# Kernel optimization log

Measured on AMD Instinct MI355X. Metric: run time of the kernel, lower is better.

## Reference

```python
import jax, jax.numpy as jnp
import numpy as np


def setup_inputs() -> dict:
    key = jax.random.key(0)
    k1, k2, k3, k4 = jax.random.split(key, 4)
    B, S, D, Y = 8, 2048, 512, 8921
    # xavier_uniform scale for [Y, D] weights
    lim = float(np.sqrt(6.0 / (Y + D)))
    x = jax.random.normal(k1, (B, S, D), dtype=jnp.float32)
    U_w = jax.random.uniform(k2, (Y, D), minval=-lim, maxval=lim, dtype=jnp.float32)
    final_w = jax.random.uniform(k3, (Y, D), minval=-lim, maxval=lim, dtype=jnp.float32)
    final_b = jax.random.normal(k4, (Y,), dtype=jnp.float32) * 0.02
    return {"x": x, "U_w": U_w, "final_w": final_w, "final_b": final_b}


def reference(x, U_w, final_w, final_b):
    # att: [B, Y, S] = U_w @ x^T
    att = jnp.einsum("yd,bsd->bys", U_w, x)
    alpha = jax.nn.softmax(att, axis=2)          # softmax over sequence
    m = jnp.einsum("bys,bsd->byd", alpha, x)      # per-label context [B, Y, D]
    y = jnp.einsum("yd,byd->by", final_w, m) + final_b  # [B, Y]
    return y
```

## Files before the change

### kernel.cpp

```cpp
#include <hip/hip_runtime.h>
#include <hip/hip_bf16.h>

constexpr int B_ = 8;
constexpr int S_ = 2048;
constexpr int D_ = 512;
constexpr int Y_ = 8921;
constexpr int MT_ = 70;
constexpr int SG_ = 4;

typedef __attribute__((ext_vector_type(8))) __bf16 bf16x8;
typedef __attribute__((ext_vector_type(4))) float f32x4;

__device__ __forceinline__ int swz_el(int row, int ksel8) {
  return row * 64 + ((ksel8 ^ row) & 7) * 8;
}

__global__ __launch_bounds__(256) void cvtW(const float* __restrict__ U,
                                            const float* __restrict__ F,
                                            __hip_bfloat16* __restrict__ wsW) {
  const int c = blockIdx.x * 256 + threadIdx.x;
  const int tile = c >> 11;
  const int row = (c >> 3) & 255;
  const int cs = c & 7;
  const int mt = tile >> 3, kt = tile & 7;
  const int ch = cs ^ (row & 7);
  const int g = row >> 5, h = (row >> 4) & 1, w = row & 15;
  const int y = mt * 128 + g * 16 + w;
  float4 f0 = {0.f, 0.f, 0.f, 0.f}, f1 = {0.f, 0.f, 0.f, 0.f};
  if (y < Y_) {
    const float* src = (h ? F : U) + (size_t)y * D_ + kt * 64 + ch * 8;
    f0 = reinterpret_cast<const float4*>(src)[0];
    f1 = reinterpret_cast<const float4*>(src)[1];
  }
  bf16x8 v;
  v[0] = (__bf16)f0.x; v[1] = (__bf16)f0.y; v[2] = (__bf16)f0.z; v[3] = (__bf16)f0.w;
  v[4] = (__bf16)f1.x; v[5] = (__bf16)f1.y; v[6] = (__bf16)f1.z; v[7] = (__bf16)f1.w;
  *reinterpret_cast<bf16x8*>(wsW + (size_t)c * 8) = v;
}

__global__ __launch_bounds__(256) void cvtX(const float* __restrict__ x,
                                            __hip_bfloat16* __restrict__ wsX) {
  const int c = blockIdx.x * 256 + threadIdx.x;
  const int lane = c & 63;
  const int idx2 = (c >> 6) & 7;
  const int wn = (c >> 9) & 3;
  const int kt = (c >> 11) & 7;
  const int st = (c >> 14) & 7;
  const int b = (c >> 17) & 7;
  const int n = idx2 >> 1, kk = idx2 & 1;
  const int s = st * 256 + wn * 64 + n * 16 + (lane & 15);
  const int k = kt * 64 + kk * 32 + (lane >> 4) * 8;
  const float* src = x + ((size_t)b * S_ + s) * D_ + k;
  const float4 f0 = reinterpret_cast<const float4*>(src)[0];
  const float4 f1 = reinterpret_cast<const float4*>(src)[1];
  bf16x8 v;
  v[0] = (__bf16)f0.x; v[1] = (__bf16)f0.y; v[2] = (__bf16)f0.z; v[3] = (__bf16)f0.w;
  v[4] = (__bf16)f1.x; v[5] = (__bf16)f1.y; v[6] = (__bf16)f1.z; v[7] = (__bf16)f1.w;
  *reinterpret_cast<bf16x8*>(wsX + (size_t)c * 8) = v;
}

__global__ __launch_bounds__(256) void zeroLN(float* __restrict__ LN, int n) {
  const int i = blockIdx.x * 256 + threadIdx.x;
  if (i < n) LN[i] = 0.f;
}

__global__ __launch_bounds__(256) void combine(const float* __restrict__ Lg,
                                               const float* __restrict__ Ng,
                                               const float* __restrict__ fb,
                                               float* __restrict__ out) {
  const int y = blockIdx.x * 256 + threadIdx.x;
  const int b = blockIdx.y;
  if (y < Y_) out[(size_t)b * Y_ + y] = Ng[b * Y_ + y] / Lg[b * Y_ + y] + fb[y];
}

typedef const __attribute__((address_space(1))) void gv_t;
typedef __attribute__((address_space(3))) void lv_t;

__device__ __forceinline__ void gld_lds16(const void* g, void* l) {
  __builtin_amdgcn_global_load_lds((gv_t*)g, (lv_t*)l, 16, 0, 0);
}

__global__ __launch_bounds__(512, 2) void pool_main(
    const __hip_bfloat16* __restrict__ wsW, const __hip_bfloat16* __restrict__ wsX,
    float* __restrict__ Lg, float* __restrict__ Ng) {
  const int bid = blockIdx.x;
  const int b = bid & 7;
  const int r = bid >> 3;
  const int mt = r % MT_;
  const int sg = r / MT_;

  const int tid = threadIdx.x;
  const int lane = tid & 63;
  const int wid = tid >> 6;
  const int wm = wid >> 2;
  const int wn = wid & 3;
  const int l15 = lane & 15;
  const int l4 = lane >> 4;

  __shared__ __bf16 ldsA[2 * 16384];
  __shared__ float redL[128];
  __shared__ float redN[128];

  if (tid < 128) { redL[tid] = 0.f; redN[tid] = 0.f; }

  const __bf16* Wbase = (const __bf16*)wsW + (size_t)mt * 8 * 16384;
  const __bf16* xc = (const __bf16*)wsX +
      ((size_t)(b * 8 + sg * 2) * 8) * 16384 + wn * 4096 + lane * 8;

  f32x4 acc[8][4];
  bf16x8 X0[4], X1[4];

  auto stageA = [&](int ktn, int par) {
    const char* src = (const char*)(Wbase + ktn * 16384) + (wid * 256 + lane) * 16;
    char* dst = (char*)ldsA + par * 32768 + wid * 4096;
#pragma unroll
    for (int i = 0; i < 4; ++i)
      gld_lds16(src + i * 1024, dst + i * 1024);
  };

  stageA(0, 0);
#pragma unroll
  for (int n = 0; n < 4; ++n)
    X0[n] = *reinterpret_cast<const bf16x8*>(xc + n * 1024);
  asm volatile("s_waitcnt vmcnt(0) lgkmcnt(0)" ::: "memory");
  __builtin_amdgcn_s_barrier();
  __builtin_amdgcn_sched_barrier(0);

  for (int si = 0; si < 2; ++si) {
#pragma unroll
    for (int m = 0; m < 8; ++m)
#pragma unroll
      for (int n = 0; n < 4; ++n) acc[m][n] = (f32x4){0.f, 0.f, 0.f, 0.f};

    for (int kt = 0; kt < 8; ++kt) {
      const __bf16* A = ldsA + ((kt & 1) << 14);
      const bool has_next = !(si == 1 && kt == 7);

      {
        bf16x8 af[4];
#pragma unroll
        for (int j = 0; j < 4; ++j)
          af[j] = *reinterpret_cast<const bf16x8*>(
              &A[swz_el(wm * 128 + j * 16 + l15, l4)]);
#pragma unroll
        for (int n = 0; n < 4; ++n)
          X1[n] = *reinterpret_cast<const bf16x8*>(xc + n * 1024 + 512);
        if (has_next) stageA((kt + 1) & 7, (kt + 1) & 1);
        __builtin_amdgcn_s_barrier();
        __builtin_amdgcn_s_setprio(1);
#pragma unroll
        for (int j = 0; j < 4; ++j)
#pragma unroll
          for (int n = 0; n < 4; ++n)
            acc[j][n] = __builtin_amdgcn_mfma_f32_16x16x32_bf16(af[j], X0[n], acc[j][n], 0, 0, 0);
        __builtin_amdgcn_s_setprio(0);
        __builtin_amdgcn_s_barrier();
      }
      {
        bf16x8 af[4];
#pragma unroll
        for (int j = 0; j < 4; ++j)
          af[j] = *reinterpret_cast<const bf16x8*>(
              &A[swz_el(wm * 128 + (4 + j) * 16 + l15, l4)]);
        __builtin_amdgcn_s_barrier();
        __builtin_amdgcn_s_setprio(1);
#pragma unroll
        for (int j = 0; j < 4; ++j)
#pragma unroll
          for (int n = 0; n < 4; ++n)
            acc[4 + j][n] = __builtin_amdgcn_mfma_f32_16x16x32_bf16(af[j], X0[n], acc[4 + j][n], 0, 0, 0);
        __builtin_amdgcn_s_setprio(0);
        __builtin_amdgcn_s_barrier();
      }
      {
        bf16x8 af[4];
#pragma unroll
        for (int j = 0; j < 4; ++j)
          af[j] = *reinterpret_cast<const bf16x8*>(
              &A[swz_el(wm * 128 + j * 16 + l15, 4 + l4)]);
        if (has_next) {
#pragma unroll
          for (int n = 0; n < 4; ++n)
            X0[n] = *reinterpret_cast<const bf16x8*>(xc + 16384 + n * 1024);
        }
        __builtin_amdgcn_s_barrier();
        __builtin_amdgcn_s_setprio(1);
#pragma unroll
        for (int j = 0; j < 4; ++j)
#pragma unroll
          for (int n = 0; n < 4; ++n)
            acc[j][n] = __builtin_amdgcn_mfma_f32_16x16x32_bf16(af[j], X1[n], acc[j][n], 0, 0, 0);
        __builtin_amdgcn_s_setprio(0);
        __builtin_amdgcn_s_barrier();
      }
      {
        bf16x8 af[4];
#pragma unroll
        for (int j = 0; j < 4; ++j)
          af[j] = *reinterpret_cast<const bf16x8*>(
              &A[swz_el(wm * 128 + (4 + j) * 16 + l15, 4 + l4)]);
        __builtin_amdgcn_s_barrier();
        __builtin_amdgcn_s_setprio(1);
#pragma unroll
        for (int j = 0; j < 4; ++j)
#pragma unroll
          for (int n = 0; n < 4; ++n)
            acc[4 + j][n] = __builtin_amdgcn_mfma_f32_16x16x32_bf16(af[j], X1[n], acc[4 + j][n], 0, 0, 0);
        __builtin_amdgcn_s_setprio(0);
        asm volatile("s_waitcnt vmcnt(0)" ::: "memory");
        __builtin_amdgcn_s_barrier();
        __builtin_amdgcn_sched_barrier(0);
      }
      xc += 16384;
    }

#pragma unroll
    for (int g = 0; g < 4; ++g)
#pragma unroll
      for (int q = 0; q < 4; ++q) {
        float l = 0.f, nn = 0.f;
#pragma unroll
        for (int n = 0; n < 4; ++n) {
          const float e = __expf(acc[2 * g][n][q]);
          l += e;
          nn = fmaf(e, acc[2 * g + 1][n][q], nn);
        }
#pragma unroll
        for (int mask = 1; mask <= 8; mask <<= 1) {
          l += __shfl_xor(l, mask);
          nn += __shfl_xor(nn, mask);
        }
        if (l15 == 0) {
          const int yl = wm * 64 + g * 16 + (l4 << 2) + q;
          atomicAdd(&redL[yl], l);
          atomicAdd(&redN[yl], nn);
        }
      }
  }

  __syncthreads();
  if (tid < 128) {
    const int y = mt * 128 + tid;
    if (y < Y_) {
      atomicAdd(&Lg[(size_t)b * Y_ + y], redL[tid]);
      atomicAdd(&Ng[(size_t)b * Y_ + y], redN[tid]);
    }
  }
}

constexpr int FB_BY = 128, FB_BS = 64, FB_BK = 64;

__device__ __forceinline__ int fswz(int row, int k) {
  return row * FB_BK + ((((k >> 3) ^ row) & 7) << 3) + (k & 7);
}

template <int CHUNKS>
__device__ __forceinline__ void fb_stage(const float* __restrict__ gbase, int rstride,
                                         int maxrow, __bf16* lds, int tid) {
#pragma unroll
  for (int i = 0; i < CHUNKS / 256; ++i) {
    const int c = tid + 256 * i;
    const int row = c >> 3;
    const int ch = c & 7;
    float4 f0 = {0.f, 0.f, 0.f, 0.f}, f1 = {0.f, 0.f, 0.f, 0.f};
    if (row < maxrow) {
      const float4* p = reinterpret_cast<const float4*>(gbase + (size_t)row * rstride + ch * 8);
      f0 = p[0]; f1 = p[1];
    }
    bf16x8 v;
    v[0] = (__bf16)f0.x; v[1] = (__bf16)f0.y; v[2] = (__bf16)f0.z; v[3] = (__bf16)f0.w;
    v[4] = (__bf16)f1.x; v[5] = (__bf16)f1.y; v[6] = (__bf16)f1.z; v[7] = (__bf16)f1.w;
    *reinterpret_cast<bf16x8*>(&lds[fswz(row, ch * 8)]) = v;
  }
}

__global__ __launch_bounds__(256) void output_layer_fallback(
    const float* __restrict__ x, const float* __restrict__ Uw,
    const float* __restrict__ Fw, const float* __restrict__ fb,
    float* __restrict__ out) {
  const int b = blockIdx.y;
  const int y0 = blockIdx.x * FB_BY;
  const int tid = threadIdx.x;
  const int lane = tid & 63;
  const int w = tid >> 6;
  const int wm = (w >> 1) * 64, wn = (w & 1) * 32;
  __shared__ __bf16 sU[FB_BY * FB_BK], sF[FB_BY * FB_BK], sX[FB_BS * FB_BK];
  float Ls[4][4], Ns[4][4];
#pragma unroll
  for (int m = 0; m < 4; ++m)
#pragma unroll
    for (int q = 0; q < 4; ++q) { Ls[m][q] = 0.f; Ns[m][q] = 0.f; }
  const float* xb = x + (size_t)b * S_ * D_;
  const int umax = Y_ - y0;
  for (int s0 = 0; s0 < S_; s0 += FB_BS) {
    f32x4 accA[4][2] = {}, accP[4][2] = {};
    for (int k0 = 0; k0 < D_; k0 += FB_BK) {
      __syncthreads();
      fb_stage<FB_BY * 8>(Uw + (size_t)y0 * D_ + k0, D_, umax, sU, tid);
      fb_stage<FB_BY * 8>(Fw + (size_t)y0 * D_ + k0, D_, umax, sF, tid);
      fb_stage<FB_BS * 8>(xb + (size_t)s0 * D_ + k0, D_, FB_BS, sX, tid);
      __syncthreads();
#pragma unroll
      for (int kk = 0; kk < 2; ++kk) {
        const int kb = kk * 32 + (lane >> 4) * 8;
        bf16x8 bx[2];
#pragma unroll
        for (int n = 0; n < 2; ++n)
          bx[n] = *reinterpret_cast<const bf16x8*>(&sX[fswz(wn + n * 16 + (lane & 15), kb)]);
#pragma unroll
        for (int m = 0; m < 4; ++m) {
          const bf16x8 aU = *reinterpret_cast<const bf16x8*>(&sU[fswz(wm + m * 16 + (lane & 15), kb)]);
          const bf16x8 aF = *reinterpret_cast<const bf16x8*>(&sF[fswz(wm + m * 16 + (lane & 15), kb)]);
#pragma unroll
          for (int n = 0; n < 2; ++n) {
            accA[m][n] = __builtin_amdgcn_mfma_f32_16x16x32_bf16(aU, bx[n], accA[m][n], 0, 0, 0);
            accP[m][n] = __builtin_amdgcn_mfma_f32_16x16x32_bf16(aF, bx[n], accP[m][n], 0, 0, 0);
          }
        }
      }
    }
#pragma unroll
    for (int m = 0; m < 4; ++m)
#pragma unroll
      for (int n = 0; n < 2; ++n)
#pragma unroll
        for (int q = 0; q < 4; ++q) {
          const float e = __expf(accA[m][n][q]);
          Ls[m][q] += e;
          Ns[m][q] = fmaf(e, accP[m][n][q], Ns[m][q]);
        }
  }
  __syncthreads();
  float* redL = reinterpret_cast<float*>(sU);
  float* redN = reinterpret_cast<float*>(sF);
  for (int i = tid; i < FB_BY; i += 256) { redL[i] = 0.f; redN[i] = 0.f; }
  __syncthreads();
#pragma unroll
  for (int m = 0; m < 4; ++m)
#pragma unroll
    for (int q = 0; q < 4; ++q) {
      float l = Ls[m][q], nn = Ns[m][q];
#pragma unroll
      for (int mask = 1; mask <= 8; mask <<= 1) {
        l += __shfl_xor(l, mask);
        nn += __shfl_xor(nn, mask);
      }
      if ((lane & 15) == 0) {
        const int yl = wm + m * 16 + ((lane >> 4) << 2) + q;
        atomicAdd(&redL[yl], l);
        atomicAdd(&redN[yl], nn);
      }
    }
  __syncthreads();
  for (int i = tid; i < FB_BY; i += 256) {
    const int y = y0 + i;
    if (y < Y_) out[(size_t)b * Y_ + y] = redN[i] / redL[i] + fb[y];
  }
}

extern "C" void kernel_launch(void* const* d_in, const int* in_sizes, int n_in,
                              void* d_out, int out_size, void* d_ws,
                              size_t ws_size, hipStream_t stream) {
  const float* x = (const float*)d_in[0];
  const float* Uw = (const float*)d_in[1];
  const float* Fw = (const float*)d_in[2];
  const float* fb = (const float*)d_in[3];
  float* out = (float*)d_out;

  constexpr size_t W_EL = (size_t)MT_ * 8 * 16384;
  constexpr size_t X_EL = (size_t)B_ * 64 * 16384;
  constexpr size_t LN_FL = (size_t)2 * B_ * Y_;
  constexpr size_t WS_NEED = (W_EL + X_EL) * 2 + LN_FL * 4;

  if (ws_size >= WS_NEED) {
    __hip_bfloat16* wsW = (__hip_bfloat16*)d_ws;
    __hip_bfloat16* wsX = wsW + W_EL;
    float* Lg = (float*)(wsX + X_EL);
    float* Ng = Lg + (size_t)B_ * Y_;

    cvtW<<<dim3((unsigned)(W_EL / 8 / 256)), dim3(256), 0, stream>>>(Uw, Fw, wsW);
    cvtX<<<dim3((unsigned)(X_EL / 8 / 256)), dim3(256), 0, stream>>>(x, wsX);
    zeroLN<<<dim3((unsigned)((LN_FL + 255) / 256)), dim3(256), 0, stream>>>(Lg, (int)LN_FL);
    pool_main<<<dim3(MT_ * B_ * SG_), dim3(512), 0, stream>>>(wsW, wsX, Lg, Ng);
    combine<<<dim3((Y_ + 255) / 256, B_), dim3(256), 0, stream>>>(Lg, Ng, fb, out);
  } else {
    output_layer_fallback<<<dim3(MT_, B_), dim3(256), 0, stream>>>(x, Uw, Fw, fb, out);
  }
}
```

Baseline: 415.9 us.

## Deepen weight staging to a four-buffer LDS pipeline with flattened loop

Replaces the double-buffered LDS staging of the weight tile with a four-buffer ring in dynamic shared memory. Three tiles are prefetched ahead, and the two sequence sub-passes are flattened into one 16-step loop, with a fold of partial sums in the middle. The wait before each barrier is relaxed to vmcnt(8) so newer loads can stay in flight, aiming to hide global-to-LDS latency. The cost is about 129KB of LDS per block, which likely allows only one 512-thread block per CU instead of two, halving occupancy.

```diff
diff --git a/kernel.cpp b/kernel.cpp
--- a/kernel.cpp
+++ b/kernel.cpp
@@ -97,11 +97,12 @@
   const int l15 = lane & 15;
   const int l4 = lane >> 4;
 
-  __shared__ __bf16 ldsA[2 * 16384];
-  __shared__ float redL[128];
-  __shared__ float redN[128];
-
-  if (tid < 128) { redL[tid] = 0.f; redN[tid] = 0.f; }
+  extern __shared__ __bf16 ldsA[];
+  float* redLN = reinterpret_cast<float*>(ldsA + 4 * 16384);
+  float* redL = redLN;
+  float* redN = redLN + 128;
+
+  if (tid < 256) redLN[tid] = 0.f;
 
   const __bf16* Wbase = (const __bf16*)wsW + (size_t)mt * 8 * 16384;
   const __bf16* xc = (const __bf16*)wsX +
@@ -110,110 +111,15 @@
   f32x4 acc[8][4];
   bf16x8 X0[4], X1[4];
 
-  auto stageA = [&](int ktn, int par) {
-    const char* src = (const char*)(Wbase + ktn * 16384) + (wid * 256 + lane) * 16;
-    char* dst = (char*)ldsA + par * 32768 + wid * 4096;
+  auto stageA = [&](int wkt, int buf) {
+    const char* src = (const char*)(Wbase + wkt * 16384) + wid * 4096 + lane * 16;
+    char* dst = (char*)ldsA + buf * 32768 + wid * 4096;
 #pragma unroll
     for (int i = 0; i < 4; ++i)
       gld_lds16(src + i * 1024, dst + i * 1024);
   };
 
-  stageA(0, 0);
-#pragma unroll
-  for (int n = 0; n < 4; ++n)
-    X0[n] = *reinterpret_cast<const bf16x8*>(xc + n * 1024);
-  asm volatile("s_waitcnt vmcnt(0) lgkmcnt(0)" ::: "memory");
-  __builtin_amdgcn_s_barrier();
-  __builtin_amdgcn_sched_barrier(0);
-
-  for (int si = 0; si < 2; ++si) {
-#pragma unroll
-    for (int m = 0; m < 8; ++m)
-#pragma unroll
-      for (int n = 0; n < 4; ++n) acc[m][n] = (f32x4){0.f, 0.f, 0.f, 0.f};
-
-    for (int kt = 0; kt < 8; ++kt) {
-      const __bf16* A = ldsA + ((kt & 1) << 14);
-      const bool has_next = !(si == 1 && kt == 7);
-
-      {
-        bf16x8 af[4];
-#pragma unroll
-        for (int j = 0; j < 4; ++j)
-          af[j] = *reinterpret_cast<const bf16x8*>(
-              &A[swz_el(wm * 128 + j * 16 + l15, l4)]);
-#pragma unroll
-        for (int n = 0; n < 4; ++n)
-          X1[n] = *reinterpret_cast<const bf16x8*>(xc + n * 1024 + 512);
-        if (has_next) stageA((kt + 1) & 7, (kt + 1) & 1);
-        __builtin_amdgcn_s_barrier();
-        __builtin_amdgcn_s_setprio(1);
-#pragma unroll
-        for (int j = 0; j < 4; ++j)
-#pragma unroll
-          for (int n = 0; n < 4; ++n)
-            acc[j][n] = __builtin_amdgcn_mfma_f32_16x16x32_bf16(af[j], X0[n], acc[j][n], 0, 0, 0);
-        __builtin_amdgcn_s_setprio(0);
-        __builtin_amdgcn_s_barrier();
-      }
-      {
-        bf16x8 af[4];
-#pragma unroll
-        for (int j = 0; j < 4; ++j)
-          af[j] = *reinterpret_cast<const bf16x8*>(
-              &A[swz_el(wm * 128 + (4 + j) * 16 + l15, l4)]);
-        __builtin_amdgcn_s_barrier();
-        __builtin_amdgcn_s_setprio(1);
-#pragma unroll
-        for (int j = 0; j < 4; ++j)
-#pragma unroll
-          for (int n = 0; n < 4; ++n)
-            acc[4 + j][n] = __builtin_amdgcn_mfma_f32_16x16x32_bf16(af[j], X0[n], acc[4 + j][n], 0, 0, 0);
-        __builtin_amdgcn_s_setprio(0);
-        __builtin_amdgcn_s_barrier();
-      }
-      {
-        bf16x8 af[4];
-#pragma unroll
-        for (int j = 0; j < 4; ++j)
-          af[j] = *reinterpret_cast<const bf16x8*>(
-              &A[swz_el(wm * 128 + j * 16 + l15, 4 + l4)]);
-        if (has_next) {
-#pragma unroll
-          for (int n = 0; n < 4; ++n)
-            X0[n] = *reinterpret_cast<const bf16x8*>(xc + 16384 + n * 1024);
-        }
-        __builtin_amdgcn_s_barrier();
-        __builtin_amdgcn_s_setprio(1);
-#pragma unroll
-        for (int j = 0; j < 4; ++j)
-#pragma unroll
-          for (int n = 0; n < 4; ++n)
-            acc[j][n] = __builtin_amdgcn_mfma_f32_16x16x32_bf16(af[j], X1[n], acc[j][n], 0, 0, 0);
-        __builtin_amdgcn_s_setprio(0);
-        __builtin_amdgcn_s_barrier();
-      }
-      {
-        bf16x8 af[4];
-#pragma unroll
-        for (int j = 0; j < 4; ++j)
-          af[j] = *reinterpret_cast<const bf16x8*>(
-              &A[swz_el(wm * 128 + (4 + j) * 16 + l15, 4 + l4)]);
-        __builtin_amdgcn_s_barrier();
-        __builtin_amdgcn_s_setprio(1);
-#pragma unroll
-        for (int j = 0; j < 4; ++j)
-#pragma unroll
-          for (int n = 0; n < 4; ++n)
-            acc[4 + j][n] = __builtin_amdgcn_mfma_f32_16x16x32_bf16(af[j], X1[n], acc[4 + j][n], 0, 0, 0);
-        __builtin_amdgcn_s_setprio(0);
-        asm volatile("s_waitcnt vmcnt(0)" ::: "memory");
-        __builtin_amdgcn_s_barrier();
-        __builtin_amdgcn_sched_barrier(0);
-      }
-      xc += 16384;
-    }
-
+  auto fold = [&]() {
 #pragma unroll
     for (int g = 0; g < 4; ++g)
 #pragma unroll
@@ -236,7 +142,108 @@
           atomicAdd(&redN[yl], nn);
         }
       }
-  }
+  };
+
+  auto zacc = [&]() {
+#pragma unroll
+    for (int m = 0; m < 8; ++m)
+#pragma unroll
+      for (int n = 0; n < 4; ++n) acc[m][n] = (f32x4){0.f, 0.f, 0.f, 0.f};
+  };
+
+  stageA(0, 0);
+  stageA(1, 1);
+  stageA(2, 2);
+#pragma unroll
+  for (int n = 0; n < 4; ++n)
+    X0[n] = *reinterpret_cast<const bf16x8*>(xc + n * 1024);
+  asm volatile("s_waitcnt vmcnt(0) lgkmcnt(0)" ::: "memory");
+  __builtin_amdgcn_s_barrier();
+  __builtin_amdgcn_sched_barrier(0);
+  zacc();
+
+  for (int t = 0; t < 16; ++t) {
+    if (t == 8) { fold(); zacc(); }
+    const __bf16* A = ldsA + (t & 3) * 16384;
+
+    {
+      bf16x8 af[4];
+#pragma unroll
+      for (int j = 0; j < 4; ++j)
+        af[j] = *reinterpret_cast<const bf16x8*>(
+            &A[swz_el(wm * 128 + j * 16 + l15, l4)]);
+#pragma unroll
+      for (int n = 0; n < 4; ++n)
+        X1[n] = *reinterpret_cast<const bf16x8*>(xc + n * 1024 + 512);
+      if (t <= 12) stageA((t + 3) & 7, (t + 3) & 3);
+      __builtin_amdgcn_s_barrier();
+      __builtin_amdgcn_s_setprio(1);
+#pragma unroll
+      for (int j = 0; j < 4; ++j)
+#pragma unroll
+        for (int n = 0; n < 4; ++n)
+          acc[j][n] = __builtin_amdgcn_mfma_f32_16x16x32_bf16(af[j], X0[n], acc[j][n], 0, 0, 0);
+      __builtin_amdgcn_s_setprio(0);
+      __builtin_amdgcn_s_barrier();
+    }
+    {
+      bf16x8 af[4];
+#pragma unroll
+      for (int j = 0; j < 4; ++j)
+        af[j] = *reinterpret_cast<const bf16x8*>(
+            &A[swz_el(wm * 128 + (4 + j) * 16 + l15, l4)]);
+      __builtin_amdgcn_s_barrier();
+      __builtin_amdgcn_s_setprio(1);
+#pragma unroll
+      for (int j = 0; j < 4; ++j)
+#pragma unroll
+        for (int n = 0; n < 4; ++n)
+          acc[4 + j][n] = __builtin_amdgcn_mfma_f32_16x16x32_bf16(af[j], X0[n], acc[4 + j][n], 0, 0, 0);
+      __builtin_amdgcn_s_setprio(0);
+      __builtin_amdgcn_s_barrier();
+    }
+    {
+      bf16x8 af[4];
+#pragma unroll
+      for (int j = 0; j < 4; ++j)
+        af[j] = *reinterpret_cast<const bf16x8*>(
+            &A[swz_el(wm * 128 + j * 16 + l15, 4 + l4)]);
+      if (t < 15) {
+#pragma unroll
+        for (int n = 0; n < 4; ++n)
+          X0[n] = *reinterpret_cast<const bf16x8*>(xc + 16384 + n * 1024);
+      }
+      __builtin_amdgcn_s_barrier();
+      __builtin_amdgcn_s_setprio(1);
+#pragma unroll
+      for (int j = 0; j < 4; ++j)
+#pragma unroll
+        for (int n = 0; n < 4; ++n)
+          acc[j][n] = __builtin_amdgcn_mfma_f32_16x16x32_bf16(af[j], X1[n], acc[j][n], 0, 0, 0);
+      __builtin_amdgcn_s_setprio(0);
+      __builtin_amdgcn_s_barrier();
+    }
+    {
+      bf16x8 af[4];
+#pragma unroll
+      for (int j = 0; j < 4; ++j)
+        af[j] = *reinterpret_cast<const bf16x8*>(
+            &A[swz_el(wm * 128 + (4 + j) * 16 + l15, 4 + l4)]);
+      __builtin_amdgcn_s_barrier();
+      __builtin_amdgcn_s_setprio(1);
+#pragma unroll
+      for (int j = 0; j < 4; ++j)
+#pragma unroll
+        for (int n = 0; n < 4; ++n)
+          acc[4 + j][n] = __builtin_amdgcn_mfma_f32_16x16x32_bf16(af[j], X1[n], acc[4 + j][n], 0, 0, 0);
+      __builtin_amdgcn_s_setprio(0);
+      asm volatile("s_waitcnt vmcnt(8)" ::: "memory");
+      __builtin_amdgcn_s_barrier();
+      __builtin_amdgcn_sched_barrier(0);
+    }
+    xc += 16384;
+  }
+  fold();
 
   __syncthreads();
   if (tid < 128) {
@@ -371,6 +378,7 @@
   constexpr size_t X_EL = (size_t)B_ * 64 * 16384;
   constexpr size_t LN_FL = (size_t)2 * B_ * Y_;
   constexpr size_t WS_NEED = (W_EL + X_EL) * 2 + LN_FL * 4;
+  constexpr int LDS_BYTES = 4 * 32768 + 1024;
 
   if (ws_size >= WS_NEED) {
     __hip_bfloat16* wsW = (__hip_bfloat16*)d_ws;
@@ -381,7 +389,10 @@
     cvtW<<<dim3((unsigned)(W_EL / 8 / 256)), dim3(256), 0, stream>>>(Uw, Fw, wsW);
     cvtX<<<dim3((unsigned)(X_EL / 8 / 256)), dim3(256), 0, stream>>>(x, wsX);
     zeroLN<<<dim3((unsigned)((LN_FL + 255) / 256)), dim3(256), 0, stream>>>(Lg, (int)LN_FL);
-    pool_main<<<dim3(MT_ * B_ * SG_), dim3(512), 0, stream>>>(wsW, wsX, Lg, Ng);
+
+    hipFuncSetAttribute((const void*)pool_main,
+                        hipFuncAttributeMaxDynamicSharedMemorySize, LDS_BYTES);
+    pool_main<<<dim3(MT_ * B_ * SG_), dim3(512), LDS_BYTES, stream>>>(wsW, wsX, Lg, Ng);
     combine<<<dim3((Y_ + 255) / 256, B_), dim3(256), 0, stream>>>(Lg, Ng, fb, out);
   } else {
     output_layer_fallback<<<dim3(MT_, B_), dim3(256), 0, stream>>>(x, Uw, Fw, fb, out);
```

New measurement: 399.7 us. -3.9%, faster.
